# Kernel tuning notes

Hardware: AMD Instinct MI355X
Metric: run time of the kernel (lower is better)

The kernel has to match this reference:

```python
import jax, jax.numpy as jnp
import numpy as np

V, E, H, K = 34, 256, 512, 256
B, T, S = 64, 200, 400


def setup_inputs() -> dict:
    key = jax.random.key(0)
    ks = jax.random.split(key, 16)
    def w(k, shape):
        return jax.random.normal(k, shape, jnp.float32) * 0.05
    z = lambda *s: jnp.zeros(s, jnp.float32)
    return {
        "target": jax.random.randint(ks[0], (T, B), 0, V).astype(jnp.int32),
        "target_mask": jnp.ones((T, B), jnp.float32),
        "attention_key": jax.random.normal(ks[1], (B, S, K), jnp.float32),
        "attention_val": jax.random.normal(ks[2], (B, S, K), jnp.float32),
        "attention_mask": jnp.ones((B, S), jnp.float32),
        "embedding": w(ks[3], (V, E)),
        "W_ih1": w(ks[4], (4 * H, E + K)), "W_hh1": w(ks[5], (4 * H, H)),
        "b_ih1": z(4 * H), "b_hh1": z(4 * H),
        "W_ih2": w(ks[6], (4 * H, H)), "W_hh2": w(ks[7], (4 * H, H)),
        "b_ih2": z(4 * H), "b_hh2": z(4 * H),
        "W_ih3": w(ks[8], (4 * H, H)), "W_hh3": w(ks[9], (4 * H, H)),
        "b_ih3": z(4 * H), "b_hh3": z(4 * H),
        "Wq": w(ks[10], (K, H)), "bq": z(K),
        "Wv": w(ks[11], (V, H)), "bv": z(V),
        "hx1": z(1, H), "cx1": z(1, H),
        "hx2": z(1, H), "cx2": z(1, H),
        "hx3": z(1, H), "cx3": z(1, H),
    }


def _lstm_cell(x, h, c, Wih, Whh, bih, bhh):
    # torch.nn.LSTMCell gate order: i, f, g, o
    g = x @ Wih.T + bih + h @ Whh.T + bhh
    i, f, gg, o = jnp.split(g, 4, axis=-1)
    c2 = jax.nn.sigmoid(f) * c + jax.nn.sigmoid(i) * jnp.tanh(gg)
    h2 = jax.nn.sigmoid(o) * jnp.tanh(c2)
    return h2, c2


def _forward(target, target_mask, attention_key, attention_val, attention_mask,
             embedding, W_ih1, W_hh1, b_ih1, b_hh1, W_ih2, W_hh2, b_ih2, b_hh2,
             W_ih3, W_hh3, b_ih3, b_hh3, Wq, bq, Wv, bv,
             hx1, cx1, hx2, cx2, hx3, cx3):
    Tlen, Bsz = target.shape
    Hd = hx1.shape[1]
    bc = lambda p: jnp.broadcast_to(p, (Bsz, Hd))
    h1, c1, h2, c2, h3, c3 = bc(hx1), bc(cx1), bc(hx2), bc(cx2), bc(hx3), bc(cx3)
    ctx = h1 @ Wq.T + bq  # initial prev_context = projection_query(hx1)
    # eval path: y_0 = 0, y_i = target[i-1]; loop runs T+1 steps (break at i==T
    # happens after logits/attention are appended but before loss).
    tokens = jnp.concatenate([jnp.zeros((1, Bsz), target.dtype), target], axis=0)

    def step(carry, y):
        h1, c1, h2, c2, h3, c3, ctx = carry
        x = jnp.concatenate([embedding[y], ctx], axis=1)  # [B, E+K]
        h1, c1 = _lstm_cell(x, h1, c1, W_ih1, W_hh1, b_ih1, b_hh1)
        h2, c2 = _lstm_cell(h1, h2, c2, W_ih2, W_hh2, b_ih2, b_hh2)
        h3, c3 = _lstm_cell(h2, h3, c3, W_ih3, W_hh3, b_ih3, b_hh3)
        q = h3 @ Wq.T + bq                                   # [B, K]
        energy = jnp.einsum('bk,bsk->bs', q, attention_key)  # [B, S]
        attn = jax.nn.softmax(energy, axis=1)
        am = attn * attention_mask
        # F.normalize(p=1): divide by max(L1 norm, 1e-12)
        an = am / jnp.maximum(jnp.sum(jnp.abs(am), axis=1, keepdims=True), 1e-12)
        new_ctx = jnp.einsum('bs,bsk->bk', an, attention_val)  # [B, K]
        logits = h3 @ Wv.T + bv                                # [B, V]
        return (h1, c1, h2, c2, h3, c3, new_ctx), (logits, attn)

    _, (logits_all, attn_all) = jax.lax.scan(step, (h1, c1, h2, c2, h3, c3, ctx), tokens)
    # CE loss (reduction='none') on first T steps, masked, summed over time, mean over batch
    logp = jax.nn.log_softmax(logits_all[:Tlen], axis=-1)            # [T, B, V]
    nll = -jnp.take_along_axis(logp, target[..., None].astype(jnp.int32), axis=-1)[..., 0]
    loss = jnp.mean(jnp.sum(nll * target_mask, axis=0))
    attn_map = attn_all[:, 0, :]  # attention map for batch element 0, [T+1, S]
    return loss, attn_map


def reference(target, target_mask, attention_key, attention_val, attention_mask,
              embedding, W_ih1, W_hh1, b_ih1, b_hh1, W_ih2, W_hh2, b_ih2, b_hh2,
              W_ih3, W_hh3, b_ih3, b_hh3, Wq, bq, Wv, bv,
              hx1, cx1, hx2, cx2, hx3, cx3):
    return _forward(target, target_mask, attention_key, attention_val, attention_mask,
                    embedding, W_ih1, W_hh1, b_ih1, b_hh1, W_ih2, W_hh2, b_ih2, b_hh2,
                    W_ih3, W_hh3, b_ih3, b_hh3, Wq, bq, Wv, bv,
                    hx1, cx1, hx2, cx2, hx3, cx3)
```

## Files before the change

### kernel.cpp

```cpp
#include <hip/hip_runtime.h>
#include <hip/hip_fp16.h>


#define BB 64
#define TT 200
#define SS 400
#define VV 34
#define EE 256
#define HH 512
#define KD 256
#define NSTEP 201
#define NWG 256
#define TPB 512

typedef unsigned long long u64;
typedef unsigned uv4 __attribute__((ext_vector_type(4)));

#define OX1   0u
#define OX2   262144u
#define OX3   524288u
#define OBS1  786432u
#define OBS2  794624u
#define OBS3  802816u
#define OWVT  811008u
#define OLACC 880640u
#define OBAR  880896u
#define OW16  1048576u
#define OWQ   13631488u
#define OKEY  13893632u
#define OVAL  27000832u

__device__ __forceinline__ void cload_x2_16(const void* p0, const void* p1,
                                            uv4& a, uv4& b) {
  asm volatile(
      "global_load_dwordx4 %0, %2, off sc0 sc1\n\t"
      "global_load_dwordx4 %1, %3, off sc0 sc1\n\t"
      "s_waitcnt vmcnt(0)"
      : "=&v"(a), "=&v"(b)
      : "v"(p0), "v"(p1)
      : "memory");
}
__device__ __forceinline__ unsigned cload_u32g(const unsigned* p) {
  unsigned v;
  asm volatile(
      "global_load_dword %0, %1, off sc0 sc1\n\t"
      "s_waitcnt vmcnt(0)"
      : "=&v"(v)
      : "v"(p)
      : "memory");
  return v;
}
__device__ __forceinline__ uv4 cload_u128(const void* p) {
  uv4 v;
  asm volatile(
      "global_load_dwordx4 %0, %1, off sc0 sc1\n\t"
      "s_waitcnt vmcnt(0)"
      : "=&v"(v)
      : "v"(p)
      : "memory");
  return v;
}
__device__ __forceinline__ void cstore_u32(void* p, unsigned v) {
  asm volatile("global_store_dword %0, %1, off sc0 sc1" ::"v"(p), "v"(v)
               : "memory");
}
__device__ __forceinline__ void cstore_u128(void* p, uv4 v) {
  asm volatile("global_store_dwordx4 %0, %1, off sc0 sc1" ::"v"(p), "v"(v)
               : "memory");
}
__device__ __forceinline__ unsigned aload_u32(const unsigned* p) {
  unsigned v;
  asm volatile(
      "global_atomic_or %0, %1, %2, off sc0 sc1\n\t"
      "s_waitcnt vmcnt(0)"
      : "=&v"(v)
      : "v"(p), "v"(0u)
      : "memory");
  return v;
}
__device__ __forceinline__ void astore_u32(unsigned* p, unsigned v) {
  __hip_atomic_exchange(p, v, __ATOMIC_RELAXED, __HIP_MEMORY_SCOPE_AGENT);
}

__device__ __forceinline__ unsigned pack2h(float a, float b) {
  return (unsigned)__half_as_ushort(__float2half(a)) |
         ((unsigned)__half_as_ushort(__float2half(b)) << 16);
}
__device__ __forceinline__ u64 pack4h(float4 v) {
  return (u64)pack2h(v.x, v.y) | ((u64)pack2h(v.z, v.w) << 32);
}
__device__ __forceinline__ float dot2acc(unsigned x, unsigned w, float acc) {
#if __has_builtin(__builtin_amdgcn_fdot2)
  typedef _Float16 h2 __attribute__((ext_vector_type(2)));
  union C { unsigned u; h2 h; };
  C a, b;
  a.u = x;
  b.u = w;
  return __builtin_amdgcn_fdot2(a.h, b.h, acc, false);
#else
  const __half2 ha = *(const __half2*)&x, hb = *(const __half2*)&w;
  const float2 fa = __half22float2(ha), fb = __half22float2(hb);
  return fmaf(fa.y, fb.y, fmaf(fa.x, fb.x, acc));
#endif
}

struct __align__(16) SM {
  union {
    union {
      u64 xs[8 * 258];
      struct { float red[256 * 17]; float gates[8 * 65]; } r;
    } l;
    struct {
      unsigned h3u[256];
      float qp[2][256];
      float qf[256];
      unsigned qh[128];
      float an[SS];
      float red[8];
      float cxp[8][256];
    } a;
    struct { float h3f[512]; float redl[VV * 8]; float lbuf[VV]; } g;
  };
  __align__(16) unsigned short hl[8][16];
};

__device__ __forceinline__ void gbar(unsigned* flags, unsigned* epoch, int wg,
                                     unsigned stamp) {
  asm volatile("s_waitcnt vmcnt(0)" ::: "memory");
  __syncthreads();
  const int tid = threadIdx.x;
  if (tid == 0) cstore_u32(flags + wg, stamp);
  if (wg == 0) {
    if (tid < 64) {
      const unsigned* p = flags + 4 * tid;
      for (;;) {
        const uv4 v = cload_u128(p);
        const bool ok = (v.x >= stamp) & (v.y >= stamp) & (v.z >= stamp) &
                        (v.w >= stamp);
        if (__all(ok)) break;
        __builtin_amdgcn_s_sleep(1);
      }
    }
    __syncthreads();
    if (tid == 0) cstore_u32(epoch, stamp);
  } else {
    if (tid == 0) {
      while (cload_u32g(epoch) < stamp) __builtin_amdgcn_s_sleep(4);
    }
  }
  __syncthreads();
}

__device__ __forceinline__ void lstm_stage(SM& sm, int cgI, int b0,
                                           const char* Xc,
                                           const unsigned short* W16,
                                           const float* __restrict__ bsum,
                                           float& creg, char* d1, int o1,
                                           char* d2, int o2) {
  const int tid = threadIdx.x;
  {
    const char* src = Xc + (size_t)b0 * 2048;
    uv4 a, b;
    cload_x2_16(src + (size_t)tid * 16, src + 8192 + (size_t)tid * 16, a, b);
    const int i0 = 2 * tid, i1 = 2 * tid + 1024;
    *(uv4*)&sm.l.xs[(i0 >> 8) * 258 + (i0 & 255)] = a;
    *(uv4*)&sm.l.xs[(i1 >> 8) * 258 + (i1 & 255)] = b;
  }
  __syncthreads();
  const int g = tid & 31, ks = tid >> 5;
  const int rg = g >> 1, bg = g & 1;
  const int R0 = ((rg >> 2) << 9) + (cgI << 4) + ((rg & 3) << 2);
  const unsigned* wb = (const unsigned*)W16;
  const unsigned* wp0 = wb + (size_t)(R0 + 0) * 512 + ks * 32;
  const unsigned* wp1 = wb + (size_t)(R0 + 1) * 512 + ks * 32;
  const unsigned* wp2 = wb + (size_t)(R0 + 2) * 512 + ks * 32;
  const unsigned* wp3 = wb + (size_t)(R0 + 3) * 512 + ks * 32;
  const unsigned* xl = (const unsigned*)sm.l.xs;
  const int xbase = bg * 4 * 516 + ks * 32;
  float acc[4][4];
#pragma unroll
  for (int i = 0; i < 4; ++i)
#pragma unroll
    for (int j = 0; j < 4; ++j) acc[i][j] = 0.f;
#pragma unroll
  for (int kk = 0; kk < 8; ++kk) {
    uv4 wv[4], xv[4];
    wv[0] = *(const uv4*)&wp0[kk * 4];
    wv[1] = *(const uv4*)&wp1[kk * 4];
    wv[2] = *(const uv4*)&wp2[kk * 4];
    wv[3] = *(const uv4*)&wp3[kk * 4];
#pragma unroll
    for (int j = 0; j < 4; ++j)
      xv[j] = *(const uv4*)&xl[xbase + j * 516 + kk * 4];
#pragma unroll
    for (int i = 0; i < 4; ++i) {
#pragma unroll
      for (int j = 0; j < 4; ++j) {
        acc[i][j] = dot2acc(xv[j].x, wv[i].x, acc[i][j]);
        acc[i][j] = dot2acc(xv[j].y, wv[i].y, acc[i][j]);
        acc[i][j] = dot2acc(xv[j].z, wv[i].z, acc[i][j]);
        acc[i][j] = dot2acc(xv[j].w, wv[i].w, acc[i][j]);
      }
    }
  }
  __syncthreads();
#pragma unroll
  for (int i = 0; i < 4; ++i)
#pragma unroll
    for (int j = 0; j < 4; ++j) acc[i][j] += __shfl_xor(acc[i][j], 32);
  if ((tid & 32) == 0) {
    const int wtid = (tid >> 6) * 32 + g;
#pragma unroll
    for (int i = 0; i < 4; ++i)
#pragma unroll
      for (int j = 0; j < 4; ++j)
        sm.l.r.red[wtid * 17 + i * 4 + j] = acc[i][j];
  }
  __syncthreads();
  {
    const int o = tid;
    const int org = o >> 5, oi = (o >> 3) & 3, obg = (o >> 2) & 1, oj = o & 3;
    const int gslot = org * 2 + obg, idx = oi * 4 + oj;
    float s = 0.f;
#pragma unroll
    for (int kp = 0; kp < 8; ++kp)
      s += sm.l.r.red[(kp * 32 + gslot) * 17 + idx];
    const int r = o >> 3, bl = o & 7;
    sm.l.r.gates[bl * 65 + r] = s;
  }
  __syncthreads();
  if (tid < 128) {
    const int bl = tid >> 4, uu = tid & 15;
    const int u = (cgI << 4) + uu;
    const float* gts = &sm.l.r.gates[bl * 65];
    const float gi = gts[uu] + bsum[u];
    const float gf = gts[16 + uu] + bsum[512 + u];
    const float gG = gts[32 + uu] + bsum[1024 + u];
    const float go = gts[48 + uu] + bsum[1536 + u];
    const float si = 1.f / (1.f + expf(-gi));
    const float sf = 1.f / (1.f + expf(-gf));
    const float so = 1.f / (1.f + expf(-go));
    const float cn = sf * creg + si * tanhf(gG);
    const float hn = so * tanhf(cn);
    creg = cn;
    sm.hl[bl][uu] = __half_as_ushort(__float2half(hn));
  }
  __syncthreads();
  if (tid < 16) {
    const int bl = tid >> 1, half = tid & 1;
    const uv4 v = *(const uv4*)&sm.hl[bl][half * 8];
    const size_t hbase = (size_t)(b0 + bl) * 1024 + (cgI << 4) + half * 8;
    cstore_u128(d1 + (hbase + o1) * 2, v);
    if (d2) cstore_u128(d2 + (hbase + o2) * 2, v);
  }
  __syncthreads();
}

__device__ __forceinline__ void attn_stage(
    SM& sm, int b, int t, const char* X3n, const unsigned short* Wq16,
    const float* __restrict__ bq, const __half* __restrict__ key16,
    const __half* __restrict__ val16, const float* __restrict__ amask,
    char* X1n, float* __restrict__ dout) {
  const int tid = threadIdx.x;
  if (tid < 64) {
    const uv4 v = cload_u128(X3n + ((size_t)b * 1024 + 512) * 2 + tid * 16);
    *(uv4*)&sm.a.h3u[tid * 4] = v;
  }
  __syncthreads();
  {
    const int c = tid & 255, kh = tid >> 8;
    const unsigned* wq = (const unsigned*)Wq16 + (size_t)c * 256 + kh * 128;
    const unsigned* hp = &sm.a.h3u[kh * 128];
    float a = 0.f;
#pragma unroll 8
    for (int i = 0; i < 32; ++i) {
      const uv4 w4 = *(const uv4*)&wq[i * 4];
      const uv4 x4 = *(const uv4*)&hp[i * 4];
      a = dot2acc(x4.x, w4.x, a);
      a = dot2acc(x4.y, w4.y, a);
      a = dot2acc(x4.z, w4.z, a);
      a = dot2acc(x4.w, w4.w, a);
    }
    sm.a.qp[kh][c] = a;
  }
  __syncthreads();
  if (tid < 256) sm.a.qf[tid] = sm.a.qp[0][tid] + sm.a.qp[1][tid] + bq[tid];
  __syncthreads();
  if (tid < 128) sm.a.qh[tid] = pack2h(sm.a.qf[2 * tid], sm.a.qf[2 * tid + 1]);
  __syncthreads();
  float e = -1e30f;
  if (tid < SS) {
    const unsigned* kp = (const unsigned*)key16 + ((size_t)b * SS + tid) * 128;
    float a = 0.f;
#pragma unroll 8
    for (int i = 0; i < 32; ++i) {
      const uv4 k4 = *(const uv4*)&kp[i * 4];
      const uv4 q4 = *(const uv4*)&sm.a.qh[i * 4];
      a = dot2acc(q4.x, k4.x, a);
      a = dot2acc(q4.y, k4.y, a);
      a = dot2acc(q4.z, k4.z, a);
      a = dot2acc(q4.w, k4.w, a);
    }
    e = a;
  }
  float m = e;
  for (int o = 32; o; o >>= 1) m = fmaxf(m, __shfl_xor(m, o));
  if ((tid & 63) == 0) sm.a.red[tid >> 6] = m;
  __syncthreads();
  m = sm.a.red[0];
#pragma unroll
  for (int i = 1; i < 8; ++i) m = fmaxf(m, sm.a.red[i]);
  __syncthreads();
  const float p = (tid < SS) ? expf(e - m) : 0.f;
  float z = p;
  for (int o = 32; o; o >>= 1) z += __shfl_xor(z, o);
  if ((tid & 63) == 0) sm.a.red[tid >> 6] = z;
  __syncthreads();
  z = 0.f;
#pragma unroll
  for (int i = 0; i < 8; ++i) z += sm.a.red[i];
  __syncthreads();
  const float at = p / z;
  if (b == 0 && tid < SS) dout[1 + (size_t)t * SS + tid] = at;
  const float am = (tid < SS) ? at * amask[(size_t)b * SS + tid] : 0.f;
  float sa = fabsf(am);
  for (int o = 32; o; o >>= 1) sa += __shfl_xor(sa, o);
  if ((tid & 63) == 0) sm.a.red[tid >> 6] = sa;
  __syncthreads();
  sa = 0.f;
#pragma unroll
  for (int i = 0; i < 8; ++i) sa += sm.a.red[i];
  const float inv = 1.f / fmaxf(sa, 1e-12f);
  if (tid < SS) sm.a.an[tid] = am * inv;
  __syncthreads();
  {
    const int kq = tid & 63, sq = tid >> 6;
    const __half* vp = val16 + ((size_t)b * SS + sq * 50) * 256 + kq * 4;
    const float* ap = &sm.a.an[sq * 50];
    float a0 = 0.f, a1 = 0.f, a2 = 0.f, a3 = 0.f;
#pragma unroll 5
    for (int s = 0; s < 50; ++s) {
      const u64 u =
          __builtin_nontemporal_load((const u64*)(vp + (size_t)s * 256));
      const unsigned lo = (unsigned)u, hi = (unsigned)(u >> 32);
      const float2 f0 = __half22float2(*(const __half2*)&lo);
      const float2 f1 = __half22float2(*(const __half2*)&hi);
      const float w = ap[s];
      a0 = fmaf(w, f0.x, a0);
      a1 = fmaf(w, f0.y, a1);
      a2 = fmaf(w, f1.x, a2);
      a3 = fmaf(w, f1.y, a3);
    }
    float* cx = &sm.a.cxp[sq][kq * 4];
    cx[0] = a0;
    cx[1] = a1;
    cx[2] = a2;
    cx[3] = a3;
  }
  __syncthreads();
  if (tid < 128) {
    float v0 = 0.f, v1 = 0.f;
#pragma unroll
    for (int i = 0; i < 8; ++i) {
      v0 += sm.a.cxp[i][2 * tid];
      v1 += sm.a.cxp[i][2 * tid + 1];
    }
    const unsigned pk = pack2h(v0, v1);
    const unsigned p1 = __shfl_down(pk, 1);
    const unsigned p2 = __shfl_down(pk, 2);
    const unsigned p3 = __shfl_down(pk, 3);
    if ((tid & 3) == 0) {
      uv4 v;
      v.x = pk;
      v.y = p1;
      v.z = p2;
      v.w = p3;
      cstore_u128(X1n + ((size_t)b * 1024 + 256 + 2 * tid) * 2, v);
    }
  }
  __syncthreads();
}

__device__ __forceinline__ void logits_stage(SM& sm, int b, int t,
                                             const char* X3n,
                                             const float* __restrict__ WvT,
                                             const float* __restrict__ bv,
                                             const int* __restrict__ target,
                                             const float* __restrict__ tmask,
                                             float& lreg) {
  const int tid = threadIdx.x;
  if (tid < 64) {
    const uv4 v = cload_u128(X3n + ((size_t)b * 1024 + 512) * 2 + tid * 16);
    const unsigned uu[4] = {v.x, v.y, v.z, v.w};
#pragma unroll
    for (int j = 0; j < 4; ++j) {
      const float2 f = __half22float2(*(const __half2*)&uu[j]);
      sm.g.h3f[tid * 8 + 2 * j] = f.x;
      sm.g.h3f[tid * 8 + 2 * j + 1] = f.y;
    }
  }
  __syncthreads();
  {
    const int c = tid & 63, ks = tid >> 6;
    if (c < VV) {
      float a = 0.f;
      const float* hp = &sm.g.h3f[ks * 64];
      const float* wp = WvT + (size_t)(ks * 64) * VV + c;
#pragma unroll 4
      for (int h = 0; h < 64; ++h) a = fmaf(hp[h], wp[h * VV], a);
      sm.g.redl[c * 8 + ks] = a;
    }
  }
  __syncthreads();
  if (tid < VV) {
    const float* rp = &sm.g.redl[tid * 8];
    float l = bv[tid];
#pragma unroll
    for (int k = 0; k < 8; ++k) l += rp[k];
    sm.g.lbuf[tid] = l;
  }
  __syncthreads();
  if (tid == 0) {
    float M = sm.g.lbuf[0];
    for (int v = 1; v < VV; ++v) M = fmaxf(M, sm.g.lbuf[v]);
    float Z = 0.f;
    for (int v = 0; v < VV; ++v) Z += expf(sm.g.lbuf[v] - M);
    const int yy = target[t * BB + b];
    lreg += tmask[t * BB + b] * (-(sm.g.lbuf[yy] - M - logf(Z)));
  }
  __syncthreads();
}

__global__ void __launch_bounds__(TPB, 1) kmain(
    const int* __restrict__ target, const float* __restrict__ tmask,
    const float* __restrict__ amask, const float* __restrict__ emb,
    const float* __restrict__ bq, const float* __restrict__ bv,
    const float* __restrict__ cx1, const float* __restrict__ cx2,
    const float* __restrict__ cx3, char* wsb, float* __restrict__ dout) {
  __shared__ SM sm;
  __shared__ int s_wid;
  const int wg = blockIdx.x, tid = threadIdx.x;
  unsigned* bar = (unsigned*)(wsb + OBAR);
  unsigned* flags = bar;
  unsigned* epoch = bar + 260;
  const unsigned short* W1 = (const unsigned short*)(wsb + OW16);
  const unsigned short* W2 = W1 + 2097152;
  const unsigned short* W3 = W2 + 2097152;
  const unsigned short* Wq16 = (const unsigned short*)(wsb + OWQ);
  const __half* key16 = (const __half*)(wsb + OKEY);
  const __half* val16 = (const __half*)(wsb + OVAL);
  const float* bs1 = (const float*)(wsb + OBS1);
  const float* bs2 = (const float*)(wsb + OBS2);
  const float* bs3 = (const float*)(wsb + OBS3);
  const float* WvT = (const float*)(wsb + OWVT);
  float* lacc = (float*)(wsb + OLACC);

  if (tid == 0) {
    unsigned xcc = 0;
    asm volatile("s_getreg_b32 %0, hwreg(20, 0, 32)" : "=s"(xcc));
    xcc &= 7u;
    unsigned* cnt = bar + 288;
    unsigned* claim = bar + 320;
    int wid = -1;
    const unsigned r = __hip_atomic_fetch_add(&cnt[xcc], 1u, __ATOMIC_RELAXED,
                                              __HIP_MEMORY_SCOPE_AGENT);
    if (r < 32u) {
      const int cand = (int)(xcc * 32u + r);
      if (__hip_atomic_exchange(&claim[cand], 1u, __ATOMIC_RELAXED,
                                __HIP_MEMORY_SCOPE_AGENT) == 0u)
        wid = cand;
    }
    for (int i = 0; wid < 0 && i < 256; ++i)
      if (__hip_atomic_exchange(&claim[i], 1u, __ATOMIC_RELAXED,
                                __HIP_MEMORY_SCOPE_AGENT) == 0u)
        wid = i;
    s_wid = wid;
  }
  __syncthreads();
  const int Wd = s_wid;
  const int xcls = Wd >> 5, lw = Wd & 31;
  const int cgI = xcls * 4 + (lw & 3);
  const int b0 = ((lw >> 2) & 7) * 8;

  float c1r = 0.f, c2r = 0.f, c3r = 0.f;
  if (tid < 128) {
    const int u = (cgI << 4) + (tid & 15);
    c1r = cx1[u];
    c2r = cx2[u];
    c3r = cx3[u];
  }
  float lreg = 0.f;
  unsigned bst = 1;

  for (int t = 0; t < NSTEP; ++t) {
    const int cur = t & 1, nxt = cur ^ 1;
    char* X1c = wsb + OX1 + (size_t)cur * 131072;
    char* X1n = wsb + OX1 + (size_t)nxt * 131072;
    char* X2c = wsb + OX2 + (size_t)cur * 131072;
    char* X2n = wsb + OX2 + (size_t)nxt * 131072;
    char* X3c = wsb + OX3 + (size_t)cur * 131072;
    char* X3n = wsb + OX3 + (size_t)nxt * 131072;

    lstm_stage(sm, cgI, b0, X1c, W1, bs1, c1r, X2c, 0, X1n, 512);
    gbar(flags, epoch, wg, bst++);
    lstm_stage(sm, cgI, b0, X2c, W2, bs2, c2r, X3c, 0, X2n, 512);
    gbar(flags, epoch, wg, bst++);
    lstm_stage(sm, cgI, b0, X3c, W3, bs3, c3r, X3n, 512, nullptr, 0);
    gbar(flags, epoch, wg, bst++);
    if (lw < 8) {
      attn_stage(sm, xcls * 8 + lw, t, X3n, Wq16, bq, key16, val16, amask,
                 X1n, dout);
    } else if (lw < 16) {
      if (t < TT)
        logits_stage(sm, xcls * 8 + lw - 8, t, X3n, WvT, bv, target, tmask,
                     lreg);
    } else if (lw < 24) {
      const int b = xcls * 8 + lw - 16;
      if (t < TT && tid < 32) {
        const int y = target[t * BB + b];
        const float4 f0 = *(const float4*)&emb[(size_t)y * EE + tid * 8];
        const float4 f1 = *(const float4*)&emb[(size_t)y * EE + tid * 8 + 4];
        const u64 lo = pack4h(f0), hi = pack4h(f1);
        uv4 v;
        v.x = (unsigned)lo;
        v.y = (unsigned)(lo >> 32);
        v.z = (unsigned)hi;
        v.w = (unsigned)(hi >> 32);
        cstore_u128(X1n + ((size_t)b * 1024 + tid * 8) * 2, v);
      }
    }
    gbar(flags, epoch, wg, bst++);
  }
  if (lw >= 8 && lw < 16 && tid == 0)
    astore_u32((unsigned*)&lacc[xcls * 8 + lw - 8], __float_as_uint(lreg));
  gbar(flags, epoch, wg, bst++);
  if (Wd == 0 && tid < 64) {
    float v = __uint_as_float(aload_u32((const unsigned*)&lacc[tid]));
    for (int o = 32; o; o >>= 1) v += __shfl_xor(v, o);
    if (tid == 0) dout[0] = v * (1.f / 64.f);
  }
}

__global__ void k_init(const float* emb, const float* Wq, const float* bq,
                       const float* Wv, const float* bih1, const float* bhh1,
                       const float* bih2, const float* bhh2, const float* bih3,
                       const float* bhh3, const float* hx1, const float* hx2,
                       const float* hx3, char* wsb) {
  const int b = blockIdx.x, tid = threadIdx.x;
  __half* X1 = (__half*)(wsb + OX1);
  __half* X2 = (__half*)(wsb + OX2);
  __half* X3 = (__half*)(wsb + OX3);
  __shared__ float hx[HH];
  for (int k = tid; k < HH; k += 256) {
    const float v = hx1[k];
    hx[k] = v;
    X1[b * 1024 + 512 + k] = __float2half(v);
    X2[b * 1024 + 512 + k] = __float2half(hx2[k]);
    X3[b * 1024 + 512 + k] = __float2half(hx3[k]);
  }
  for (int k = tid; k < EE; k += 256) X1[b * 1024 + k] = __float2half(emb[k]);
  __syncthreads();
  for (int c = tid; c < KD; c += 256) {
    float a = bq[c];
    for (int k = 0; k < HH; ++k) a = fmaf(hx[k], Wq[(size_t)c * HH + k], a);
    X1[b * 1024 + 256 + c] = __float2half(a);
  }
  if (b == 0) {
    float* s1 = (float*)(wsb + OBS1);
    float* s2 = (float*)(wsb + OBS2);
    float* s3 = (float*)(wsb + OBS3);
    for (int i = tid; i < 2048; i += 256) {
      s1[i] = bih1[i] + bhh1[i];
      s2[i] = bih2[i] + bhh2[i];
      s3[i] = bih3[i] + bhh3[i];
    }
    float* wvt = (float*)(wsb + OWVT);
    for (int i = tid; i < HH * VV; i += 256) {
      const int h = i / VV, v = i % VV;
      wvt[i] = Wv[(size_t)v * HH + h];
    }
    float* lacc = (float*)(wsb + OLACC);
    for (int i = tid; i < 64; i += 256) lacc[i] = 0.f;
    unsigned* bar = (unsigned*)(wsb + OBAR);
    for (int i = tid; i < 1024; i += 256) bar[i] = 0u;
  }
}

__global__ void k_cvt(const float* key, const float* val, const float* Wq,
                      const float* Wih1, const float* Whh1, const float* Wih2,
                      const float* Whh2, const float* Wih3, const float* Whh3,
                      char* wsb) {
  const int blk = blockIdx.x, tid = threadIdx.x;
  if (blk < 6144) {
    const int layer = blk >> 11, R = blk & 2047;
    const float* Wih = (layer == 0) ? Wih1 : ((layer == 1) ? Wih2 : Wih3);
    const float* Whh = (layer == 0) ? Whh1 : ((layer == 1) ? Whh2 : Whh3);
    __half* dst = (__half*)(wsb + OW16) + (size_t)layer * 2097152 +
                  (size_t)R * 1024;
    const int k0 = tid * 4;
    const float* src = (k0 < 512) ? &Wih[(size_t)R * 512 + k0]
                                  : &Whh[(size_t)R * 512 + (k0 - 512)];
    const float4 v = *(const float4*)src;
    dst[k0 + 0] = __float2half(v.x);
    dst[k0 + 1] = __float2half(v.y);
    dst[k0 + 2] = __float2half(v.z);
    dst[k0 + 3] = __float2half(v.w);
  } else if (blk < 7744) {
    const size_t base = (size_t)(blk - 6144) * 4096 + (size_t)tid * 16;
    __half* dst = (__half*)(wsb + OKEY);
#pragma unroll
    for (int j = 0; j < 4; ++j) {
      const float4 v = *(const float4*)&key[base + j * 4];
      dst[base + j * 4 + 0] = __float2half(v.x);
      dst[base + j * 4 + 1] = __float2half(v.y);
      dst[base + j * 4 + 2] = __float2half(v.z);
      dst[base + j * 4 + 3] = __float2half(v.w);
    }
  } else if (blk < 9344) {
    const size_t base = (size_t)(blk - 7744) * 4096 + (size_t)tid * 16;
    __half* dst = (__half*)(wsb + OVAL);
#pragma unroll
    for (int j = 0; j < 4; ++j) {
      const float4 v = *(const float4*)&val[base + j * 4];
      dst[base + j * 4 + 0] = __float2half(v.x);
      dst[base + j * 4 + 1] = __float2half(v.y);
      dst[base + j * 4 + 2] = __float2half(v.z);
      dst[base + j * 4 + 3] = __float2half(v.w);
    }
  } else {
    const size_t base = (size_t)(blk - 9344) * 4096 + (size_t)tid * 16;
    __half* dst = (__half*)(wsb + OWQ);
#pragma unroll
    for (int j = 0; j < 4; ++j) {
      const float4 v = *(const float4*)&Wq[base + j * 4];
      dst[base + j * 4 + 0] = __float2half(v.x);
      dst[base + j * 4 + 1] = __float2half(v.y);
      dst[base + j * 4 + 2] = __float2half(v.z);
      dst[base + j * 4 + 3] = __float2half(v.w);
    }
  }
}

extern "C" void kernel_launch(void* const* d_in, const int* in_sizes, int n_in,
                              void* d_out, int out_size, void* d_ws,
                              size_t ws_size, hipStream_t stream) {
  const int* target = (const int*)d_in[0];
  const float* tmask = (const float*)d_in[1];
  const float* key = (const float*)d_in[2];
  const float* val = (const float*)d_in[3];
  const float* amask = (const float*)d_in[4];
  const float* emb = (const float*)d_in[5];
  const float* Wih1 = (const float*)d_in[6];
  const float* Whh1 = (const float*)d_in[7];
  const float* bih1 = (const float*)d_in[8];
  const float* bhh1 = (const float*)d_in[9];
  const float* Wih2 = (const float*)d_in[10];
  const float* Whh2 = (const float*)d_in[11];
  const float* bih2 = (const float*)d_in[12];
  const float* bhh2 = (const float*)d_in[13];
  const float* Wih3 = (const float*)d_in[14];
  const float* Whh3 = (const float*)d_in[15];
  const float* bih3 = (const float*)d_in[16];
  const float* bhh3 = (const float*)d_in[17];
  const float* Wq = (const float*)d_in[18];
  const float* bq = (const float*)d_in[19];
  const float* Wv = (const float*)d_in[20];
  const float* bv = (const float*)d_in[21];
  const float* hx1 = (const float*)d_in[22];
  const float* cx1 = (const float*)d_in[23];
  const float* hx2 = (const float*)d_in[24];
  const float* cx2 = (const float*)d_in[25];
  const float* hx3 = (const float*)d_in[26];
  const float* cx3 = (const float*)d_in[27];
  float* out = (float*)d_out;
  char* wsb = (char*)d_ws;

  hipLaunchKernelGGL(k_init, dim3(64), dim3(256), 0, stream, emb, Wq, bq, Wv,
                     bih1, bhh1, bih2, bhh2, bih3, bhh3, hx1, hx2, hx3, wsb);
  hipLaunchKernelGGL(k_cvt, dim3(9376), dim3(256), 0, stream, key, val, Wq,
                     Wih1, Whh1, Wih2, Whh2, Wih3, Whh3, wsb);

  void* args[] = {(void*)&target, (void*)&tmask, (void*)&amask, (void*)&emb,
                  (void*)&bq,     (void*)&bv,    (void*)&cx1,   (void*)&cx2,
                  (void*)&cx3,    (void*)&wsb,   (void*)&out};
  hipLaunchCooperativeKernel((const void*)kmain, dim3(NWG), dim3(TPB), args, 0,
                             stream);
}
```

Baseline: 10.04 ms.

## Repartition LSTM stage work across workgroups as 64 units by 2 batches

```diff
diff --git a/kernel.cpp b/kernel.cpp
--- a/kernel.cpp
+++ b/kernel.cpp
@@ -30,16 +30,6 @@
 #define OKEY  13893632u
 #define OVAL  27000832u
 
-__device__ __forceinline__ void cload_x2_16(const void* p0, const void* p1,
-                                            uv4& a, uv4& b) {
-  asm volatile(
-      "global_load_dwordx4 %0, %2, off sc0 sc1\n\t"
-      "global_load_dwordx4 %1, %3, off sc0 sc1\n\t"
-      "s_waitcnt vmcnt(0)"
-      : "=&v"(a), "=&v"(b)
-      : "v"(p0), "v"(p1)
-      : "memory");
-}
 __device__ __forceinline__ unsigned cload_u32g(const unsigned* p) {
   unsigned v;
   asm volatile(
@@ -106,10 +96,7 @@
 
 struct __align__(16) SM {
   union {
-    union {
-      u64 xs[8 * 258];
-      struct { float red[256 * 17]; float gates[8 * 65]; } r;
-    } l;
+    struct { unsigned xsm[2][512]; float gates[2][4][64]; } l;
     struct {
       unsigned h3u[256];
       float qp[2][256];
@@ -121,7 +108,7 @@
     } a;
     struct { float h3f[512]; float redl[VV * 8]; float lbuf[VV]; } g;
   };
-  __align__(16) unsigned short hl[8][16];
+  __align__(16) unsigned short hl[2][64];
 };
 
 __device__ __forceinline__ void gbar(unsigned* flags, unsigned* epoch, int wg,
@@ -151,105 +138,59 @@
   __syncthreads();
 }
 
-__device__ __forceinline__ void lstm_stage(SM& sm, int cgI, int b0,
+__device__ __forceinline__ void lstm_stage(SM& sm, int ubase, int b0,
                                            const char* Xc,
                                            const unsigned short* W16,
                                            const float* __restrict__ bsum,
                                            float& creg, char* d1, int o1,
                                            char* d2, int o2) {
   const int tid = threadIdx.x;
+  if (tid < 256) {
+    const int bb = tid >> 7, off = tid & 127;
+    const uv4 v = cload_u128(Xc + ((size_t)(b0 + bb) * 1024) * 2 + off * 16);
+    *(uv4*)&sm.l.xsm[bb][off * 4] = v;
+  }
+  __syncthreads();
   {
-    const char* src = Xc + (size_t)b0 * 2048;
-    uv4 a, b;
-    cload_x2_16(src + (size_t)tid * 16, src + 8192 + (size_t)tid * 16, a, b);
-    const int i0 = 2 * tid, i1 = 2 * tid + 1024;
-    *(uv4*)&sm.l.xs[(i0 >> 8) * 258 + (i0 & 255)] = a;
-    *(uv4*)&sm.l.xs[(i1 >> 8) * 258 + (i1 & 255)] = b;
-  }
-  __syncthreads();
-  const int g = tid & 31, ks = tid >> 5;
-  const int rg = g >> 1, bg = g & 1;
-  const int R0 = ((rg >> 2) << 9) + (cgI << 4) + ((rg & 3) << 2);
-  const unsigned* wb = (const unsigned*)W16;
-  const unsigned* wp0 = wb + (size_t)(R0 + 0) * 512 + ks * 32;
-  const unsigned* wp1 = wb + (size_t)(R0 + 1) * 512 + ks * 32;
-  const unsigned* wp2 = wb + (size_t)(R0 + 2) * 512 + ks * 32;
-  const unsigned* wp3 = wb + (size_t)(R0 + 3) * 512 + ks * 32;
-  const unsigned* xl = (const unsigned*)sm.l.xs;
-  const int xbase = bg * 4 * 516 + ks * 32;
-  float acc[4][4];
-#pragma unroll
-  for (int i = 0; i < 4; ++i)
-#pragma unroll
-    for (int j = 0; j < 4; ++j) acc[i][j] = 0.f;
-#pragma unroll
-  for (int kk = 0; kk < 8; ++kk) {
-    uv4 wv[4], xv[4];
-    wv[0] = *(const uv4*)&wp0[kk * 4];
-    wv[1] = *(const uv4*)&wp1[kk * 4];
-    wv[2] = *(const uv4*)&wp2[kk * 4];
-    wv[3] = *(const uv4*)&wp3[kk * 4];
-#pragma unroll
-    for (int j = 0; j < 4; ++j)
-      xv[j] = *(const uv4*)&xl[xbase + j * 516 + kk * 4];
-#pragma unroll
-    for (int i = 0; i < 4; ++i) {
-#pragma unroll
-      for (int j = 0; j < 4; ++j) {
-        acc[i][j] = dot2acc(xv[j].x, wv[i].x, acc[i][j]);
-        acc[i][j] = dot2acc(xv[j].y, wv[i].y, acc[i][j]);
-        acc[i][j] = dot2acc(xv[j].z, wv[i].z, acc[i][j]);
-        acc[i][j] = dot2acc(xv[j].w, wv[i].w, acc[i][j]);
-      }
-    }
-  }
-  __syncthreads();
-#pragma unroll
-  for (int i = 0; i < 4; ++i)
-#pragma unroll
-    for (int j = 0; j < 4; ++j) acc[i][j] += __shfl_xor(acc[i][j], 32);
-  if ((tid & 32) == 0) {
-    const int wtid = (tid >> 6) * 32 + g;
-#pragma unroll
-    for (int i = 0; i < 4; ++i)
-#pragma unroll
-      for (int j = 0; j < 4; ++j)
-        sm.l.r.red[wtid * 17 + i * 4 + j] = acc[i][j];
-  }
-  __syncthreads();
-  {
-    const int o = tid;
-    const int org = o >> 5, oi = (o >> 3) & 3, obg = (o >> 2) & 1, oj = o & 3;
-    const int gslot = org * 2 + obg, idx = oi * 4 + oj;
-    float s = 0.f;
-#pragma unroll
-    for (int kp = 0; kp < 8; ++kp)
-      s += sm.l.r.red[(kp * 32 + gslot) * 17 + idx];
-    const int r = o >> 3, bl = o & 7;
-    sm.l.r.gates[bl * 65 + r] = s;
+    const int b = tid & 1, r = tid >> 1;
+    const int g = r >> 6, ul = r & 63;
+    const int u = ubase + ul;
+    const unsigned* wrow =
+        (const unsigned*)W16 + (size_t)(g * 512 + u) * 512;
+    const unsigned* xrow = &sm.l.xsm[b][0];
+    float a0 = 0.f, a1 = 0.f, a2 = 0.f, a3 = 0.f;
+#pragma unroll 4
+    for (int k = 0; k < 128; ++k) {
+      const uv4 w4 = *(const uv4*)&wrow[k * 4];
+      const uv4 x4 = *(const uv4*)&xrow[k * 4];
+      a0 = dot2acc(x4.x, w4.x, a0);
+      a1 = dot2acc(x4.y, w4.y, a1);
+      a2 = dot2acc(x4.z, w4.z, a2);
+      a3 = dot2acc(x4.w, w4.w, a3);
+    }
+    sm.l.gates[b][g][ul] = (a0 + a1) + (a2 + a3);
   }
   __syncthreads();
   if (tid < 128) {
-    const int bl = tid >> 4, uu = tid & 15;
-    const int u = (cgI << 4) + uu;
-    const float* gts = &sm.l.r.gates[bl * 65];
-    const float gi = gts[uu] + bsum[u];
-    const float gf = gts[16 + uu] + bsum[512 + u];
-    const float gG = gts[32 + uu] + bsum[1024 + u];
-    const float go = gts[48 + uu] + bsum[1536 + u];
+    const int bb = tid >> 6, uu = tid & 63;
+    const int gu = ubase + uu;
+    const float gi = sm.l.gates[bb][0][uu] + bsum[gu];
+    const float gf = sm.l.gates[bb][1][uu] + bsum[512 + gu];
+    const float gG = sm.l.gates[bb][2][uu] + bsum[1024 + gu];
+    const float go = sm.l.gates[bb][3][uu] + bsum[1536 + gu];
     const float si = 1.f / (1.f + expf(-gi));
     const float sf = 1.f / (1.f + expf(-gf));
     const float so = 1.f / (1.f + expf(-go));
     const float cn = sf * creg + si * tanhf(gG);
     const float hn = so * tanhf(cn);
     creg = cn;
-    sm.hl[bl][uu] = __half_as_ushort(__float2half(hn));
+    sm.hl[bb][uu] = __half_as_ushort(__float2half(hn));
   }
   __syncthreads();
   if (tid < 16) {
-    const int bl = tid >> 1, half = tid & 1;
-    const uv4 v = *(const uv4*)&sm.hl[bl][half * 8];
-    const size_t hbase = (size_t)(b0 + bl) * 1024 + (cgI << 4) + half * 8;
+    const int bb = tid >> 3, seg = tid & 7;
+    const uv4 v = *(const uv4*)&sm.hl[bb][seg * 8];
+    const size_t hbase = (size_t)(b0 + bb) * 1024 + ubase + seg * 8;
     cstore_u128(d1 + (hbase + o1) * 2, v);
     if (d2) cstore_u128(d2 + (hbase + o2) * 2, v);
   }
@@ -479,12 +420,12 @@
   __syncthreads();
   const int Wd = s_wid;
   const int xcls = Wd >> 5, lw = Wd & 31;
-  const int cgI = xcls * 4 + (lw & 3);
-  const int b0 = ((lw >> 2) & 7) * 8;
+  const int ubase = xcls * 64;
+  const int b0 = lw * 2;
 
   float c1r = 0.f, c2r = 0.f, c3r = 0.f;
   if (tid < 128) {
-    const int u = (cgI << 4) + (tid & 15);
+    const int u = ubase + (tid & 63);
     c1r = cx1[u];
     c2r = cx2[u];
     c3r = cx3[u];
@@ -501,11 +442,11 @@
     char* X3c = wsb + OX3 + (size_t)cur * 131072;
     char* X3n = wsb + OX3 + (size_t)nxt * 131072;
 
-    lstm_stage(sm, cgI, b0, X1c, W1, bs1, c1r, X2c, 0, X1n, 512);
+    lstm_stage(sm, ubase, b0, X1c, W1, bs1, c1r, X2c, 0, X1n, 512);
     gbar(flags, epoch, wg, bst++);
-    lstm_stage(sm, cgI, b0, X2c, W2, bs2, c2r, X3c, 0, X2n, 512);
+    lstm_stage(sm, ubase, b0, X2c, W2, bs2, c2r, X3c, 0, X2n, 512);
     gbar(flags, epoch, wg, bst++);
-    lstm_stage(sm, cgI, b0, X3c, W3, bs3, c3r, X3n, 512, nullptr, 0);
+    lstm_stage(sm, ubase, b0, X3c, W3, bs3, c3r, X3n, 512, nullptr, 0);
     gbar(flags, epoch, wg, bst++);
     if (lw < 8) {
       attn_stage(sm, xcls * 8 + lw, t, X3n, Wq16, bq, key16, val16, amask,
```

After: 15.37 ms. 53.1% more time.
